# Kernel tuning notes

Hardware: AMD Instinct MI355X
Metric: run time of the kernel (lower is better)

The kernel has to match this reference:

```python
import jax, jax.numpy as jnp
import numpy as np

N_NODES = 100000
N_EDGES = 1600000
D = 64
N_LAYERS = 3  # 1 input EdgeConv + hidden_layers(=2)
N_GRAPHS = 32
N_CLASSES = 40


def setup_inputs() -> dict:
    key = jax.random.key(0)
    ks = jax.random.split(key, 12)
    h = jax.random.normal(ks[0], (N_NODES, D), dtype=jnp.float32)
    src = jax.random.randint(ks[1], (N_EDGES,), 0, N_NODES, dtype=jnp.int32)
    dst = jax.random.randint(ks[2], (N_EDGES,), 0, N_NODES, dtype=jnp.int32)
    graph_ids = jnp.sort(jax.random.randint(ks[3], (N_NODES,), 0, N_GRAPHS, dtype=jnp.int32))
    s = 0.05
    theta_w = jax.random.normal(ks[4], (N_LAYERS, D, D), dtype=jnp.float32) * s
    theta_b = jax.random.normal(ks[5], (N_LAYERS, D), dtype=jnp.float32) * s
    phi_w = jax.random.normal(ks[6], (N_LAYERS, D, D), dtype=jnp.float32) * s
    phi_b = jax.random.normal(ks[7], (N_LAYERS, D), dtype=jnp.float32) * s
    cls_w = jax.random.normal(ks[8], (D, N_CLASSES), dtype=jnp.float32) * s
    cls_b = jax.random.normal(ks[9], (N_CLASSES,), dtype=jnp.float32) * s
    return {"h": h, "src": src, "dst": dst, "graph_ids": graph_ids,
            "theta_w": theta_w, "theta_b": theta_b, "phi_w": phi_w, "phi_b": phi_b,
            "cls_w": cls_w, "cls_b": cls_b}


def _edgeconv(h, src, dst, tw, tb, pw, pb):
    # DGL EdgeConv: h_i = max_{j in N(i)} Theta(x_j - x_i) + Phi(x_i)
    # Linearity: Theta(x_j - x_i) = (x@Theta)[j] - (x@Theta)[i]
    t = h @ tw  # [N, D]
    p = h @ pw + (tb + pb)  # fold both biases in
    msg = t[src] - t[dst] + p[dst]  # [E, D] edge messages
    agg = jax.ops.segment_max(msg, dst, num_segments=h.shape[0])
    has_in = jax.ops.segment_sum(jnp.ones((dst.shape[0],), h.dtype), dst,
                                 num_segments=h.shape[0]) > 0
    return jnp.where(has_in[:, None], agg, jnp.zeros_like(agg))  # DGL zero-fill


def reference(h, src, dst, graph_ids, theta_w, theta_b, phi_w, phi_b, cls_w, cls_b):
    # forward never applies batch_norms; dropout is identity at inference
    for l in range(N_LAYERS):
        h = _edgeconv(h, src, dst, theta_w[l], theta_b[l], phi_w[l], phi_b[l])
    # MaxPooling readout over nodes of each graph
    hg = jax.ops.segment_max(h, graph_ids, num_segments=N_GRAPHS)  # [G, D]
    return hg @ cls_w + cls_b  # [G, n_classes]
```

## Files before the change

### kernel.cpp

```cpp
#include <hip/hip_runtime.h>
#include <hip/hip_bf16.h>
#include <climits>

#define N_NODES   100000
#define N_EDGES   1600000
#define D         64
#define N_GRAPHS  32
#define N_CLASSES 40
#define N_TILES   (N_NODES / 16)
#define TPW       2
#define GEMM_WAVES ((N_TILES + TPW - 1) / TPW)
#define GEMM_BLOCKS ((GEMM_WAVES + 3) / 4)

#define BKT_SHIFT 7
#define BKT_NODES 128
#define NB        ((N_NODES + BKT_NODES - 1) / BKT_NODES)
#define CHUNK     4096
#define NCHUNK    ((N_EDGES + CHUNK - 1) / CHUNK)
#define EPT       (CHUNK / 256)

typedef _Float16 f16_t;
typedef f16_t f16x8 __attribute__((ext_vector_type(8)));
typedef f16_t f16x4 __attribute__((ext_vector_type(4)));
typedef float  f32x4  __attribute__((ext_vector_type(4)));

__device__ __forceinline__ int f2ord(float f) {
    int i = __float_as_int(f);
    return (i >= 0) ? i : (i ^ 0x7FFFFFFF);
}
__device__ __forceinline__ float ord2f(int i) {
    int j = (i >= 0) ? i : (i ^ 0x7FFFFFFF);
    return __int_as_float(j);
}

__global__ __launch_bounds__(256) void k_prep(
    const float* __restrict__ tw, const float* __restrict__ pw,
    const float* __restrict__ tb, const float* __restrict__ pb,
    f16_t* __restrict__ wcat, float* __restrict__ bcat,
    int* __restrict__ bktcnt, int* __restrict__ hg)
{
    const int i = blockIdx.x * 256 + threadIdx.x;
    if (i < 3 * 128 * 64) {
        const int l = i >> 13;
        const int rem = i & 8191;
        const int n = rem >> 6;
        const int k = rem & 63;
        const float v = (n < D) ? tw[l * 4096 + k * D + n] : pw[l * 4096 + k * D + (n - D)];
        wcat[i] = (f16_t)v;
    }
    if (i < 3 * D) bcat[i] = tb[i] + pb[i];
    if (i < NB) bktcnt[i] = 0;
    if (i < N_GRAPHS * D) hg[i] = INT_MIN;
}

__global__ __launch_bounds__(256) void k_gemm0_hist(
    const float* __restrict__ hf,
    const f16_t* __restrict__ wcat, const float* __restrict__ bcat,
    f16_t* __restrict__ t, f16_t* __restrict__ q,
    const int* __restrict__ dst, int* __restrict__ bktcnt)
{
    __shared__ int l[NB];
    if (blockIdx.x >= GEMM_BLOCKS) {
        const int bb = blockIdx.x - GEMM_BLOCKS;
        for (int i = threadIdx.x; i < NB; i += 256) l[i] = 0;
        __syncthreads();
        const int base = bb * CHUNK;
        #pragma unroll
        for (int i = 0; i < EPT; ++i) {
            const int e = base + i * 256 + threadIdx.x;
            if (e < N_EDGES) atomicAdd(&l[dst[e] >> BKT_SHIFT], 1);
        }
        __syncthreads();
        for (int i = threadIdx.x; i < NB; i += 256)
            if (l[i]) atomicAdd(&bktcnt[i], l[i]);
        return;
    }
    const int lane = threadIdx.x & 63;
    const int wid  = blockIdx.x * 4 + (threadIdx.x >> 6);
    const int r16  = lane & 15;
    const int kg   = lane >> 4;
    const int koff = kg * 8;

    f16x8 bfrag[8][2];
    #pragma unroll
    for (int c = 0; c < 8; ++c)
        #pragma unroll
        for (int s = 0; s < 2; ++s)
            bfrag[c][s] = *(const f16x8*)&wcat[(c * 16 + r16) * D + s * 32 + koff];

    f32x4 bias4[4];
    #pragma unroll
    for (int c = 0; c < 4; ++c) bias4[c] = *(const f32x4*)&bcat[c * 16 + kg * 4];

    #pragma unroll
    for (int tt = 0; tt < TPW; ++tt) {
        const int tile = wid * TPW + tt;
        if (tile >= N_TILES) return;
        const long rowbase = (long)tile * 16;
        const long arow = rowbase + r16;

        f16x8 afrag[2];
        #pragma unroll
        for (int s = 0; s < 2; ++s) {
            const f32x4 v0 = *(const f32x4*)&hf[arow * D + s * 32 + koff];
            const f32x4 v1 = *(const f32x4*)&hf[arow * D + s * 32 + koff + 4];
            f16x8 a;
            a[0] = (f16_t)v0[0]; a[1] = (f16_t)v0[1];
            a[2] = (f16_t)v0[2]; a[3] = (f16_t)v0[3];
            a[4] = (f16_t)v1[0]; a[5] = (f16_t)v1[1];
            a[6] = (f16_t)v1[2]; a[7] = (f16_t)v1[3];
            afrag[s] = a;
        }

        const f32x4 zero = {0.0f, 0.0f, 0.0f, 0.0f};
        f32x4 acc[8];
        #pragma unroll
        for (int c = 0; c < 8; ++c) {
            acc[c] = __builtin_amdgcn_mfma_f32_16x16x32_f16(bfrag[c][0], afrag[0], zero, 0, 0, 0);
            acc[c] = __builtin_amdgcn_mfma_f32_16x16x32_f16(bfrag[c][1], afrag[1], acc[c], 0, 0, 0);
        }

        const long node = rowbase + r16;
        #pragma unroll
        for (int c = 0; c < 4; ++c) {
            f16x4 tv, qv;
            #pragma unroll
            for (int j = 0; j < 4; ++j) {
                const float tf = acc[c][j];
                tv[j] = (f16_t)tf;
                qv[j] = (f16_t)(acc[c + 4][j] - tf + bias4[c][j]);
            }
            *(f16x4*)&t[node * D + c * 16 + kg * 4] = tv;
            *(f16x4*)&q[node * D + c * 16 + kg * 4] = qv;
        }
    }
}


__global__ __launch_bounds__(256) void k_bkt_scan(
    const int* __restrict__ bktcnt, int* __restrict__ boff, int* __restrict__ gcur,
    int* __restrict__ rowptr)
{
    __shared__ int s[256];
    const int t = threadIdx.x;
    int v[4], sum = 0;
    #pragma unroll
    for (int i = 0; i < 4; ++i) {
        const int idx = t * 4 + i;
        v[i] = (idx < NB) ? bktcnt[idx] : 0;
        sum += v[i];
    }
    s[t] = sum;
    __syncthreads();
    #pragma unroll
    for (int off = 1; off < 256; off <<= 1) {
        int x = (t >= off) ? s[t - off] : 0;
        __syncthreads();
        s[t] += x;
        __syncthreads();
    }
    int run = s[t] - sum;
    #pragma unroll
    for (int i = 0; i < 4; ++i) {
        const int idx = t * 4 + i;
        if (idx < NB) {
            boff[idx] = run;
            gcur[idx] = run;
        }
        run += v[i];
    }
    if (t == 255) {
        boff[NB] = N_EDGES;
        rowptr[N_NODES] = N_EDGES;
    }
}

__global__ __launch_bounds__(256) void k_bkt_scatter(
    const int* __restrict__ src, const int* __restrict__ dst,
    int* __restrict__ gcur, unsigned* __restrict__ bke)
{
    __shared__ int lcnt[NB];
    __shared__ int gb[NB];
    for (int i = threadIdx.x; i < NB; i += 256) lcnt[i] = 0;
    __syncthreads();
    const int base = blockIdx.x * CHUNK;
    unsigned pk[EPT], br[EPT];
    #pragma unroll
    for (int i = 0; i < EPT; ++i) {
        const int e = base + i * 256 + threadIdx.x;
        if (e < N_EDGES) {
            const int d = dst[e];
            const int b = d >> BKT_SHIFT;
            const int r = atomicAdd(&lcnt[b], 1);
            pk[i] = ((unsigned)(d & (BKT_NODES - 1)) << 17) | (unsigned)src[e];
            br[i] = ((unsigned)b << 13) | (unsigned)r;
        } else {
            br[i] = 0xFFFFFFFFu;
        }
    }
    __syncthreads();
    for (int i = threadIdx.x; i < NB; i += 256) {
        const int c = lcnt[i];
        gb[i] = c ? atomicAdd(&gcur[i], c) : 0;
    }
    __syncthreads();
    #pragma unroll
    for (int i = 0; i < EPT; ++i) {
        if (br[i] != 0xFFFFFFFFu) {
            const int b = br[i] >> 13;
            const int r = br[i] & 8191;
            bke[gb[b] + r] = pk[i];
        }
    }
}

__global__ __launch_bounds__(256) void k_bkt_sort(
    const int* __restrict__ boff, const unsigned* __restrict__ bke,
    int* __restrict__ ebuf, int* __restrict__ rowptr)
{
    __shared__ int cnt[BKT_NODES];
    __shared__ int pfx[BKT_NODES];
    const int b = blockIdx.x;
    const int tid = threadIdx.x;
    const int beg = boff[b];
    const int end = boff[b + 1];

    if (tid < BKT_NODES) cnt[tid] = 0;
    __syncthreads();
    for (int e = beg + tid; e < end; e += 256)
        atomicAdd(&cnt[bke[e] >> 17], 1);
    __syncthreads();
    if (tid < BKT_NODES) pfx[tid] = cnt[tid];
    __syncthreads();
    #pragma unroll
    for (int off = 1; off < BKT_NODES; off <<= 1) {
        int x = 0;
        if (tid < BKT_NODES && tid >= off) x = pfx[tid - off];
        __syncthreads();
        if (tid < BKT_NODES) pfx[tid] += x;
        __syncthreads();
    }
    if (tid < BKT_NODES) {
        const int excl = pfx[tid] - cnt[tid];
        const int node = b * BKT_NODES + tid;
        if (node <= N_NODES) rowptr[node] = beg + excl;
        cnt[tid] = beg + excl;
    }
    __syncthreads();
    for (int e = beg + tid; e < end; e += 256) {
        const unsigned pk = bke[e];
        const int pos = atomicAdd(&cnt[pk >> 17], 1);
        ebuf[pos] = (int)(pk & 0x1FFFFu);
    }
}

__global__ __launch_bounds__(256) void k_gemm_mfma(
    const f16_t* __restrict__ hb,
    const f16_t* __restrict__ wcat,
    const float* __restrict__ bcat,
    f16_t* __restrict__ t, f16_t* __restrict__ q)
{
    const int lane = threadIdx.x & 63;
    const int wid  = blockIdx.x * 4 + (threadIdx.x >> 6);
    const int r16  = lane & 15;
    const int kg   = lane >> 4;
    const int koff = kg * 8;

    f16x8 bfrag[8][2];
    #pragma unroll
    for (int c = 0; c < 8; ++c)
        #pragma unroll
        for (int s = 0; s < 2; ++s)
            bfrag[c][s] = *(const f16x8*)&wcat[(c * 16 + r16) * D + s * 32 + koff];

    f32x4 bias4[4];
    #pragma unroll
    for (int c = 0; c < 4; ++c) bias4[c] = *(const f32x4*)&bcat[c * 16 + kg * 4];

    #pragma unroll
    for (int tt = 0; tt < TPW; ++tt) {
        const int tile = wid * TPW + tt;
        if (tile >= N_TILES) return;
        const long rowbase = (long)tile * 16;
        const long arow = rowbase + r16;

        f16x8 afrag[2];
        afrag[0] = *(const f16x8*)&hb[arow * D + koff];
        afrag[1] = *(const f16x8*)&hb[arow * D + 32 + koff];

        const f32x4 zero = {0.0f, 0.0f, 0.0f, 0.0f};
        f32x4 acc[8];
        #pragma unroll
        for (int c = 0; c < 8; ++c) {
            acc[c] = __builtin_amdgcn_mfma_f32_16x16x32_f16(bfrag[c][0], afrag[0], zero, 0, 0, 0);
            acc[c] = __builtin_amdgcn_mfma_f32_16x16x32_f16(bfrag[c][1], afrag[1], acc[c], 0, 0, 0);
        }

        const long node = rowbase + r16;
        #pragma unroll
        for (int c = 0; c < 4; ++c) {
            f16x4 tv, qv;
            #pragma unroll
            for (int j = 0; j < 4; ++j) {
                const float tf = acc[c][j];
                tv[j] = (f16_t)tf;
                qv[j] = (f16_t)(acc[c + 4][j] - tf + bias4[c][j]);
            }
            *(f16x4*)&t[node * D + c * 16 + kg * 4] = tv;
            *(f16x4*)&q[node * D + c * 16 + kg * 4] = qv;
        }
    }
}

__global__ __launch_bounds__(256) void k_edge_csr(
    const int* __restrict__ rowptr, const int* __restrict__ ebuf,
    const f16_t* __restrict__ t, const f16_t* __restrict__ q,
    f16_t* __restrict__ agg)
{
    const int lane = threadIdx.x & 63;
    const int grp  = lane >> 3;
    const int g    = lane & 7;
    const int node = (blockIdx.x * 4 + (threadIdx.x >> 6)) * 8 + grp;
    const int beg = rowptr[node];
    const int end = rowptr[node + 1];
    const long nrow = (long)node * D + g * 8;

    if (end == beg) {
        f16x8 z;
        #pragma unroll
        for (int i = 0; i < 8; ++i) z[i] = (f16_t)0.0f;
        *(f16x8*)&agg[nrow] = z;
        return;
    }

    const f16x8 qv = *(const f16x8*)&q[nrow];
    const int last = end - 1;
    f16x8 m0, m1;
    {
        int r[8];
        #pragma unroll
        for (int u = 0; u < 8; ++u) r[u] = ebuf[min(beg + u, last)];
        f16x8 v[8];
        #pragma unroll
        for (int u = 0; u < 8; ++u) v[u] = *(const f16x8*)&t[((long)r[u] << 6) + g * 8];
        m0 = __builtin_elementwise_max(__builtin_elementwise_max(v[0], v[1]),
                                       __builtin_elementwise_max(v[2], v[3]));
        m1 = __builtin_elementwise_max(__builtin_elementwise_max(v[4], v[5]),
                                       __builtin_elementwise_max(v[6], v[7]));
    }
    for (int e0 = beg + 8; e0 < end; e0 += 8) {
        int r[8];
        #pragma unroll
        for (int u = 0; u < 8; ++u) r[u] = ebuf[min(e0 + u, last)];
        f16x8 v[8];
        #pragma unroll
        for (int u = 0; u < 8; ++u) v[u] = *(const f16x8*)&t[((long)r[u] << 6) + g * 8];
        m0 = __builtin_elementwise_max(m0,
                 __builtin_elementwise_max(__builtin_elementwise_max(v[0], v[1]),
                                           __builtin_elementwise_max(v[2], v[3])));
        m1 = __builtin_elementwise_max(m1,
                 __builtin_elementwise_max(__builtin_elementwise_max(v[4], v[5]),
                                           __builtin_elementwise_max(v[6], v[7])));
    }
    const f16x8 m = __builtin_elementwise_max(m0, m1);
    *(f16x8*)&agg[nrow] = m + qv;
}

__global__ __launch_bounds__(256) void k_pool(
    const f16_t* __restrict__ agg, const int* __restrict__ gid,
    int* __restrict__ hg)
{
    __shared__ int hl[N_GRAPHS * D];
    for (int i = threadIdx.x; i < N_GRAPHS * D; i += 256) hl[i] = INT_MIN;
    __syncthreads();

    const int lane = threadIdx.x & 63;
    const int wv   = threadIdx.x >> 6;
    const int n0 = (blockIdx.x * 4 + wv) * 32;
    if (n0 < N_NODES) {
        const int nend = (n0 + 32 < N_NODES) ? n0 + 32 : N_NODES;
        int cur = gid[n0];
        float m = -INFINITY;
        for (int n = n0; n < nend; ++n) {
            const int g = gid[n];
            if (g != cur) {
                atomicMax(&hl[cur * D + lane], f2ord(m));
                cur = g;
                m = -INFINITY;
            }
            m = fmaxf(m, (float)agg[(long)n * D + lane]);
        }
        atomicMax(&hl[cur * D + lane], f2ord(m));
    }
    __syncthreads();

    const int blo = blockIdx.x * 128;
    const int bhi = (blo + 127 < N_NODES - 1) ? blo + 127 : N_NODES - 1;
    const int glo = gid[blo];
    const int ghi = gid[bhi];
    const int cnt = (ghi - glo + 1) * D;
    for (int i = threadIdx.x; i < cnt; i += 256) {
        const int v = hl[glo * D + i];
        if (v != INT_MIN) atomicMax(&hg[glo * D + i], v);
    }
}

__global__ __launch_bounds__(256) void k_cls(
    const int* __restrict__ hg, const float* __restrict__ w,
    const float* __restrict__ b, float* __restrict__ out)
{
    __shared__ float s_h[N_GRAPHS * D];
    __shared__ float s_w[D * N_CLASSES];
    __shared__ float s_b[N_CLASSES];
    for (int i = threadIdx.x; i < N_GRAPHS * D; i += 256) s_h[i] = ord2f(hg[i]);
    for (int i = threadIdx.x; i < D * N_CLASSES; i += 256) s_w[i] = w[i];
    if (threadIdx.x < N_CLASSES) s_b[threadIdx.x] = b[threadIdx.x];
    __syncthreads();
    for (int o = threadIdx.x; o < N_GRAPHS * N_CLASSES; o += 256) {
        const int g = o / N_CLASSES;
        const int c = o % N_CLASSES;
        float acc = s_b[c];
        #pragma unroll
        for (int k = 0; k < D; ++k)
            acc = fmaf(s_h[g * D + k], s_w[k * N_CLASSES + c], acc);
        out[o] = acc;
    }
}

extern "C" void kernel_launch(void* const* d_in, const int* in_sizes, int n_in,
                              void* d_out, int out_size, void* d_ws, size_t ws_size,
                              hipStream_t stream) {
    const float* h       = (const float*)d_in[0];
    const int*   src     = (const int*)d_in[1];
    const int*   dst     = (const int*)d_in[2];
    const int*   gid     = (const int*)d_in[3];
    const float* theta_w = (const float*)d_in[4];
    const float* theta_b = (const float*)d_in[5];
    const float* phi_w   = (const float*)d_in[6];
    const float* phi_b   = (const float*)d_in[7];
    const float* cls_w   = (const float*)d_in[8];
    const float* cls_b   = (const float*)d_in[9];
    float* out = (float*)d_out;

    const size_t NF = (size_t)N_NODES * D;
    char* p = (char*)d_ws;
    f16_t* t     = (f16_t*)p;   p += NF * 2;
    f16_t* q     = (f16_t*)p;   p += NF * 2;
    f16_t* agg   = (f16_t*)p;   p += NF * 2;
    f16_t* wcat  = (f16_t*)p;   p += 3 * 128 * D * 2;
    float*  bcat = (float*)p;   p += 3 * D * 4;
    unsigned* bke = (unsigned*)p; p += (size_t)N_EDGES * 4;
    int* ebuf    = (int*)p;     p += (size_t)N_EDGES * 4;
    int* rowptr  = (int*)p;     p += (N_NODES + 1) * 4;
    int* bktcnt  = (int*)p;     p += NB * 4;
    int* boff    = (int*)p;     p += (NB + 1) * 4;
    int* gcur    = (int*)p;     p += NB * 4;
    int* hg      = (int*)p;     p += N_GRAPHS * D * 4;
    const size_t need = (size_t)(p - (char*)d_ws);
    if (ws_size < need) {
        hipMemsetAsync(d_out, 0, (size_t)out_size * sizeof(float), stream);
        return;
    }

    const int EDGE_GRID = N_NODES / 32;
    const int POOL_GRID = (N_NODES + 127) / 128;

    k_prep<<<96, 256, 0, stream>>>(theta_w, phi_w, theta_b, phi_b, wcat, bcat, bktcnt, hg);

    k_gemm0_hist<<<GEMM_BLOCKS + NCHUNK, 256, 0, stream>>>(h, wcat, bcat, t, q, dst, bktcnt);

    k_bkt_scan<<<1, 256, 0, stream>>>(bktcnt, boff, gcur, rowptr);
    k_bkt_scatter<<<NCHUNK, 256, 0, stream>>>(src, dst, gcur, bke);
    k_bkt_sort<<<NB, 256, 0, stream>>>(boff, bke, ebuf, rowptr);

    k_edge_csr<<<EDGE_GRID, 256, 0, stream>>>(rowptr, ebuf, t, q, agg);

    k_gemm_mfma<<<GEMM_BLOCKS, 256, 0, stream>>>(agg, wcat + 128 * D, bcat + D, t, q);
    k_edge_csr<<<EDGE_GRID, 256, 0, stream>>>(rowptr, ebuf, t, q, agg);

    k_gemm_mfma<<<GEMM_BLOCKS, 256, 0, stream>>>(agg, wcat + 2 * 128 * D, bcat + 2 * D, t, q);
    k_edge_csr<<<EDGE_GRID, 256, 0, stream>>>(rowptr, ebuf, t, q, agg);

    k_pool<<<POOL_GRID, 256, 0, stream>>>(agg, gid, hg);
    k_cls<<<1, 256, 0, stream>>>(hg, cls_w, cls_b, out);
}
```

Before: 240.4 us.

## Fuse edge max-aggregation with next layer's MFMA GEMM via shared memory

```diff
diff --git a/kernel.cpp b/kernel.cpp
--- a/kernel.cpp
+++ b/kernel.cpp
@@ -254,61 +254,101 @@
     }
 }
 
-__global__ __launch_bounds__(256) void k_gemm_mfma(
-    const f16_t* __restrict__ hb,
-    const f16_t* __restrict__ wcat,
-    const float* __restrict__ bcat,
-    f16_t* __restrict__ t, f16_t* __restrict__ q)
-{
+__global__ __launch_bounds__(256) void k_edge_gemm(
+    const int* __restrict__ rowptr, const int* __restrict__ ebuf,
+    const f16_t* __restrict__ t_in, const f16_t* __restrict__ q_in,
+    const f16_t* __restrict__ wcat_next, const float* __restrict__ bcat_next,
+    f16_t* __restrict__ t_out, f16_t* __restrict__ q_out)
+{
+    __shared__ f16_t sAgg[32 * D];
     const int lane = threadIdx.x & 63;
-    const int wid  = blockIdx.x * 4 + (threadIdx.x >> 6);
+    const int wv   = threadIdx.x >> 6;
+    const int grp  = lane >> 3;
+    const int g    = lane & 7;
+    const int ln   = wv * 8 + grp;
+    const int node = blockIdx.x * 32 + ln;
+
     const int r16  = lane & 15;
     const int kg   = lane >> 4;
     const int koff = kg * 8;
-
-    f16x8 bfrag[8][2];
-    #pragma unroll
-    for (int c = 0; c < 8; ++c)
-        #pragma unroll
-        for (int s = 0; s < 2; ++s)
-            bfrag[c][s] = *(const f16x8*)&wcat[(c * 16 + r16) * D + s * 32 + koff];
-
-    f32x4 bias4[4];
-    #pragma unroll
-    for (int c = 0; c < 4; ++c) bias4[c] = *(const f32x4*)&bcat[c * 16 + kg * 4];
-
-    #pragma unroll
-    for (int tt = 0; tt < TPW; ++tt) {
-        const int tile = wid * TPW + tt;
-        if (tile >= N_TILES) return;
-        const long rowbase = (long)tile * 16;
-        const long arow = rowbase + r16;
-
-        f16x8 afrag[2];
-        afrag[0] = *(const f16x8*)&hb[arow * D + koff];
-        afrag[1] = *(const f16x8*)&hb[arow * D + 32 + koff];
-
-        const f32x4 zero = {0.0f, 0.0f, 0.0f, 0.0f};
-        f32x4 acc[8];
-        #pragma unroll
-        for (int c = 0; c < 8; ++c) {
-            acc[c] = __builtin_amdgcn_mfma_f32_16x16x32_f16(bfrag[c][0], afrag[0], zero, 0, 0, 0);
-            acc[c] = __builtin_amdgcn_mfma_f32_16x16x32_f16(bfrag[c][1], afrag[1], acc[c], 0, 0, 0);
-        }
-
-        const long node = rowbase + r16;
-        #pragma unroll
-        for (int c = 0; c < 4; ++c) {
-            f16x4 tv, qv;
+    const int cbase = (wv & 1) * 2;
+    f16x8 bfrag[4][2];
+    #pragma unroll
+    for (int i = 0; i < 2; ++i)
+        #pragma unroll
+        for (int s = 0; s < 2; ++s) {
+            bfrag[i][s]     = *(const f16x8*)&wcat_next[((cbase + i) * 16 + r16) * D + s * 32 + koff];
+            bfrag[i + 2][s] = *(const f16x8*)&wcat_next[((cbase + i + 4) * 16 + r16) * D + s * 32 + koff];
+        }
+    f32x4 bias4[2];
+    #pragma unroll
+    for (int i = 0; i < 2; ++i) bias4[i] = *(const f32x4*)&bcat_next[(cbase + i) * 16 + kg * 4];
+
+    const int beg = rowptr[node];
+    const int end = rowptr[node + 1];
+    f16x8 o;
+    if (end == beg) {
+        #pragma unroll
+        for (int i = 0; i < 8; ++i) o[i] = (f16_t)0.0f;
+    } else {
+        const f16x8 qv = *(const f16x8*)&q_in[(long)node * D + g * 8];
+        const int last = end - 1;
+        f16x8 m0, m1;
+        {
+            int r[8];
             #pragma unroll
-            for (int j = 0; j < 4; ++j) {
-                const float tf = acc[c][j];
-                tv[j] = (f16_t)tf;
-                qv[j] = (f16_t)(acc[c + 4][j] - tf + bias4[c][j]);
-            }
-            *(f16x4*)&t[node * D + c * 16 + kg * 4] = tv;
-            *(f16x4*)&q[node * D + c * 16 + kg * 4] = qv;
-        }
+            for (int u = 0; u < 8; ++u) r[u] = ebuf[min(beg + u, last)];
+            f16x8 v[8];
+            #pragma unroll
+            for (int u = 0; u < 8; ++u) v[u] = *(const f16x8*)&t_in[((long)r[u] << 6) + g * 8];
+            m0 = __builtin_elementwise_max(__builtin_elementwise_max(v[0], v[1]),
+                                           __builtin_elementwise_max(v[2], v[3]));
+            m1 = __builtin_elementwise_max(__builtin_elementwise_max(v[4], v[5]),
+                                           __builtin_elementwise_max(v[6], v[7]));
+        }
+        for (int e0 = beg + 8; e0 < end; e0 += 8) {
+            int r[8];
+            #pragma unroll
+            for (int u = 0; u < 8; ++u) r[u] = ebuf[min(e0 + u, last)];
+            f16x8 v[8];
+            #pragma unroll
+            for (int u = 0; u < 8; ++u) v[u] = *(const f16x8*)&t_in[((long)r[u] << 6) + g * 8];
+            m0 = __builtin_elementwise_max(m0,
+                     __builtin_elementwise_max(__builtin_elementwise_max(v[0], v[1]),
+                                               __builtin_elementwise_max(v[2], v[3])));
+            m1 = __builtin_elementwise_max(m1,
+                     __builtin_elementwise_max(__builtin_elementwise_max(v[4], v[5]),
+                                               __builtin_elementwise_max(v[6], v[7])));
+        }
+        o = __builtin_elementwise_max(m0, m1) + qv;
+    }
+    *(f16x8*)&sAgg[ln * D + g * 8] = o;
+    __syncthreads();
+
+    const int nt = wv >> 1;
+    f16x8 afrag[2];
+    afrag[0] = *(const f16x8*)&sAgg[(nt * 16 + r16) * D + koff];
+    afrag[1] = *(const f16x8*)&sAgg[(nt * 16 + r16) * D + 32 + koff];
+
+    const long nodeB = (long)blockIdx.x * 32 + nt * 16 + r16;
+    const f32x4 zero = {0.0f, 0.0f, 0.0f, 0.0f};
+    #pragma unroll
+    for (int i = 0; i < 2; ++i) {
+        f32x4 acc_t, acc_p;
+        acc_t = __builtin_amdgcn_mfma_f32_16x16x32_f16(bfrag[i][0],     afrag[0], zero,  0, 0, 0);
+        acc_t = __builtin_amdgcn_mfma_f32_16x16x32_f16(bfrag[i][1],     afrag[1], acc_t, 0, 0, 0);
+        acc_p = __builtin_amdgcn_mfma_f32_16x16x32_f16(bfrag[i + 2][0], afrag[0], zero,  0, 0, 0);
+        acc_p = __builtin_amdgcn_mfma_f32_16x16x32_f16(bfrag[i + 2][1], afrag[1], acc_p, 0, 0, 0);
+        const int c = cbase + i;
+        f16x4 tv, qv2;
+        #pragma unroll
+        for (int j = 0; j < 4; ++j) {
+            const float tf = acc_t[j];
+            tv[j]  = (f16_t)tf;
+            qv2[j] = (f16_t)(acc_p[j] - tf + bias4[i][j]);
+        }
+        *(f16x4*)&t_out[nodeB * D + c * 16 + kg * 4] = tv;
+        *(f16x4*)&q_out[nodeB * D + c * 16 + kg * 4] = qv2;
     }
 }
 
@@ -444,8 +484,10 @@
 
     const size_t NF = (size_t)N_NODES * D;
     char* p = (char*)d_ws;
-    f16_t* t     = (f16_t*)p;   p += NF * 2;
-    f16_t* q     = (f16_t*)p;   p += NF * 2;
+    f16_t* t1    = (f16_t*)p;   p += NF * 2;
+    f16_t* q1    = (f16_t*)p;   p += NF * 2;
+    f16_t* t2    = (f16_t*)p;   p += NF * 2;
+    f16_t* q2    = (f16_t*)p;   p += NF * 2;
     f16_t* agg   = (f16_t*)p;   p += NF * 2;
     f16_t* wcat  = (f16_t*)p;   p += 3 * 128 * D * 2;
     float*  bcat = (float*)p;   p += 3 * D * 4;
@@ -462,24 +504,23 @@
         return;
     }
 
-    const int EDGE_GRID = N_NODES / 32;
+    const int FUSE_GRID = N_NODES / 32;
     const int POOL_GRID = (N_NODES + 127) / 128;
 
     k_prep<<<96, 256, 0, stream>>>(theta_w, phi_w, theta_b, phi_b, wcat, bcat, bktcnt, hg);
 
-    k_gemm0_hist<<<GEMM_BLOCKS + NCHUNK, 256, 0, stream>>>(h, wcat, bcat, t, q, dst, bktcnt);
+    k_gemm0_hist<<<GEMM_BLOCKS + NCHUNK, 256, 0, stream>>>(h, wcat, bcat, t1, q1, dst, bktcnt);
 
     k_bkt_scan<<<1, 256, 0, stream>>>(bktcnt, boff, gcur, rowptr);
     k_bkt_scatter<<<NCHUNK, 256, 0, stream>>>(src, dst, gcur, bke);
     k_bkt_sort<<<NB, 256, 0, stream>>>(boff, bke, ebuf, rowptr);
 
-    k_edge_csr<<<EDGE_GRID, 256, 0, stream>>>(rowptr, ebuf, t, q, agg);
-
-    k_gemm_mfma<<<GEMM_BLOCKS, 256, 0, stream>>>(agg, wcat + 128 * D, bcat + D, t, q);
-    k_edge_csr<<<EDGE_GRID, 256, 0, stream>>>(rowptr, ebuf, t, q, agg);
-
-    k_gemm_mfma<<<GEMM_BLOCKS, 256, 0, stream>>>(agg, wcat + 2 * 128 * D, bcat + 2 * D, t, q);
-    k_edge_csr<<<EDGE_GRID, 256, 0, stream>>>(rowptr, ebuf, t, q, agg);
+    k_edge_gemm<<<FUSE_GRID, 256, 0, stream>>>(
+        rowptr, ebuf, t1, q1, wcat + 128 * D, bcat + D, t2, q2);
+    k_edge_gemm<<<FUSE_GRID, 256, 0, stream>>>(
+        rowptr, ebuf, t2, q2, wcat + 2 * 128 * D, bcat + 2 * D, t1, q1);
+
+    k_edge_csr<<<FUSE_GRID, 256, 0, stream>>>(rowptr, ebuf, t1, q1, agg);
 
     k_pool<<<POOL_GRID, 256, 0, stream>>>(agg, gid, hg);
     k_cls<<<1, 256, 0, stream>>>(hg, cls_w, cls_b, out);
```

After: 219.2 us. 1.1x faster.
